# Kernel tuning notes

Hardware: AMD Instinct MI355X
Metric: run time of the kernel (lower is better)

## Reference

```python
import jax, jax.numpy as jnp
import numpy as np
from jax import lax

IOU_THRESHOLD = 0.1
B, N = 4, 8192


def setup_inputs() -> dict:
    key = jax.random.key(0)
    # [B, 5, N]: rows 0..3 = cx, cy, w, h; row 4 = confidence score in (0, 1)
    outputs = jax.random.uniform(key, (B, 5, N), dtype=jnp.float32)
    return {"outputs": outputs}


def _nms_single(p):
    """Greedy NMS on one image. p: [5, N] -> [5, N] with kept boxes
    compacted to the front (original column order preserved) and the rest
    zero-padded. Matches the torch loop: repeatedly take the highest-scoring
    surviving box, drop all boxes with IoU >= threshold (box keeps itself),
    and drop boxes with score <= 0."""
    boxes, scores = p[:4], p[4]
    n = scores.shape[0]
    order = jnp.argsort(-scores)            # descending score order
    b = boxes[:, order]

    x1 = b[0] - b[2] * 0.5
    y1 = b[1] - b[3] * 0.5
    x2 = b[0] + b[2] * 0.5
    y2 = b[1] + b[3] * 0.5
    area = (x2 - x1) * (y2 - y1)

    iw = jnp.clip(jnp.minimum(x2[:, None], x2[None, :]) - jnp.maximum(x1[:, None], x1[None, :]), 0.0)
    ih = jnp.clip(jnp.minimum(y2[:, None], y2[None, :]) - jnp.maximum(y1[:, None], y1[None, :]), 0.0)
    inter = iw * ih
    union = area[:, None] + area[None, :] - inter
    iou = inter / (union + 1e-8)            # [N, N] in sorted order

    idx_range = jnp.arange(n)
    keep_init = scores[order] > 0           # non_zero_scores filter

    def body(i, keep):
        # if box i (in score order) survives, suppress j with IoU >= thr, j != i
        row_keep = (iou[i] < IOU_THRESHOLD) | (idx_range == i)
        return jnp.where(keep[i], keep & row_keep, keep)

    keep_sorted = lax.fori_loop(0, n, body, keep_init)

    # map keep mask back to original column order
    keep_orig = jnp.zeros((n,), bool).at[order].set(keep_sorted)
    # stable compaction: kept columns first, original relative order preserved
    perm = jnp.argsort(jnp.where(keep_orig, 0, 1), stable=True)
    gathered = p[:, perm]                    # [5, N]
    valid = idx_range < jnp.sum(keep_orig)
    return jnp.where(valid[None, :], gathered, 0.0)


def reference(outputs):
    # torch version pads to the max detections across the batch; here we keep
    # the fixed width N (extra columns are zero), same kept values/order.
    return jax.vmap(_nms_single)(outputs)


if __name__ == "__main__":
    inp = setup_inputs()
    out = jax.jit(reference)(**inp)
    print(out.shape, out.dtype)
```

## Files before the change

### kernel.cpp

```cpp
#include <hip/hip_runtime.h>

#pragma clang fp contract(off)

#define NBOX 8192
#define BLK  1024
#define EPT  8
#define NBUCK 2048
#define NB 256
#define IOU_THR 0.1f

typedef unsigned short u16;
typedef unsigned int u32;
typedef unsigned long long u64;

#define MND 0x1.999999p-4

#define SMEM_TOT 160896

__global__ __launch_bounds__(BLK, 4) void nms_kernel(const float* __restrict__ in,
                                                     float* __restrict__ out) {
    __shared__ __align__(16) char smem[SMEM_TOT];
    const int img = blockIdx.x;
    const float* __restrict__ p = in + (size_t)img * 5 * NBOX;
    float* __restrict__ o = out + (size_t)img * 5 * NBOX;
    const int t = threadIdx.x;
    const int lane = t & 63;
    const int wid = t >> 6;

    float4* box   = (float4*)smem;
    u16* A        = (u16*)(smem + 131072);
    float4* bx    = (float4*)(smem + 147456);
    u64 (*mat)[4] = (u64(*)[4])(smem + 151552);
    float4* kx    = (float4*)(smem + 151552);
    u32* pfxA     = (u32*)(smem + 155648);
    u32* kom      = (u32*)(smem + 159744);
    int* wcnt     = (int*)(smem + 160768);
    u64* keptQ    = (u64*)(smem + 160832);
    int* S0sh     = (int*)(smem + 160864);
    u64* skey  = (u64*)smem;
    u32* hist  = (u32*)(smem + 65536);
    u32* bbase = (u32*)(smem + 73728);

    for (int i = t; i < NBUCK; i += BLK) hist[i] = 0;
    if (t < 256) kom[t] = 0;
    if (t == 0) *S0sh = 0;
    __syncthreads();

    u32 mybkt[EPT], myarr[EPT], mykeyhi[EPT];
#pragma unroll
    for (int e = 0; e < EPT; e++) {
        int j = t + e * BLK;
        float s = p[4 * NBOX + j];
        u32 u = __float_as_uint(s);
        u32 ordb = u ^ (u32)(((int)u >> 31) | (int)0x80000000);
        mykeyhi[e] = ~ordb;
        int vb = (int)(s * (float)NBUCK);
        vb = vb < 0 ? 0 : (vb > NBUCK - 1 ? NBUCK - 1 : vb);
        mybkt[e] = (u32)(NBUCK - 1 - vb);
        myarr[e] = atomicAdd(&hist[mybkt[e]], 1u);
        u64 bal = __ballot(s > 0.0f);
        if (lane == 0) atomicAdd(S0sh, (int)__popcll(bal));
    }
    __syncthreads();

    {
        u32 h0 = hist[2 * t], h1 = hist[2 * t + 1];
        int v = (int)(h0 + h1);
        int x = v;
        for (int d = 1; d < 64; d <<= 1) {
            int y = __shfl_up(x, d, 64);
            if (lane >= d) x += y;
        }
        if (lane == 63) wcnt[wid] = x;
        __syncthreads();
        int wb = 0;
        for (int i = 0; i < wid; i++) wb += wcnt[i];
        int excl = wb + x - v;
        bbase[2 * t] = (u32)excl;
        bbase[2 * t + 1] = (u32)excl + h0;
    }
    __syncthreads();

#pragma unroll
    for (int e = 0; e < EPT; e++) {
        u32 pos = bbase[mybkt[e]] + myarr[e];
        skey[pos] = ((u64)mykeyhi[e] << 32) | (u32)(t + e * BLK);
    }
    __syncthreads();

#pragma unroll
    for (int e = 0; e < EPT; e++) {
        u32 b = mybkt[e];
        u32 lo = bbase[b], hi2 = lo + hist[b];
        u64 me = ((u64)mykeyhi[e] << 32) | (u32)(t + e * BLK);
        u32 r = lo;
        for (u32 q = lo; q < hi2; q++) r += (skey[q] < me) ? 1u : 0u;
        A[r] = (u16)(t + e * BLK);
    }
    __syncthreads();
    int S = *S0sh;

#pragma unroll
    for (int e = 0; e < EPT; e++) {
        int j = t + e * BLK;
        float cx = p[j], cy = p[NBOX + j];
        float w_ = p[2 * NBOX + j], h_ = p[3 * NBOX + j];
        box[j] = make_float4(cx - w_ * 0.5f, cy - h_ * 0.5f,
                             cx + w_ * 0.5f, cy + h_ * 0.5f);
    }
    __syncthreads();

    if (t < NB) bx[t] = box[A[t]];
    __syncthreads();

    while (S > 0) {
        int nb = S < NB ? S : NB;

        {
            int i = t >> 2, ws = t & 3;
            if (i < nb) {
                float4 bi = bx[i];
                float ari = (bi.z - bi.x) * (bi.w - bi.y);
                u64 bits = 0;
                int c0 = ws * 64;
                int cmax = nb - c0; if (cmax > 64) cmax = 64;
                for (int cc = 0; cc < cmax; cc++) {
                    float4 bc = bx[c0 + cc];
                    float arc = (bc.z - bc.x) * (bc.w - bc.y);
                    float iw = fmaxf(fminf(bi.z, bc.z) - fmaxf(bi.x, bc.x), 0.0f);
                    float ih = fmaxf(fminf(bi.w, bc.w) - fmaxf(bi.y, bc.y), 0.0f);
                    float inter = iw * ih;
                    float t1 = ari + arc;
                    float t2 = t1 - inter;
                    float u  = t2 + 1e-8f;
                    if ((double)inter > MND * (double)u) bits |= (1ull << cc);
                }
                if (i >= c0 && i < c0 + 64) bits &= ~(1ull << (i - c0));
                mat[i][ws] = bits;
            }
        }
        __syncthreads();

        if (wid == 0) {
            u64 r0[4], r1[4], r2[4], r3[4];
#pragma unroll
            for (int wq = 0; wq < 4; wq++) {
                r0[wq] = mat[lane][wq];
                r1[wq] = mat[64 + lane][wq];
                r2[wq] = mat[128 + lane][wq];
                r3[wq] = mat[192 + lane][wq];
            }
            u64 A0, A1, A2, A3;
            {
                int n0 = nb;       A0 = n0 <= 0 ? 0ull : (n0 >= 64 ? ~0ull : ((1ull << n0) - 1ull));
                int n1 = nb - 64;  A1 = n1 <= 0 ? 0ull : (n1 >= 64 ? ~0ull : ((1ull << n1) - 1ull));
                int n2 = nb - 128; A2 = n2 <= 0 ? 0ull : (n2 >= 64 ? ~0ull : ((1ull << n2) - 1ull));
                int n3 = nb - 192; A3 = n3 <= 0 ? 0ull : (n3 >= 64 ? ~0ull : ((1ull << n3) - 1ull));
            }
            u64 K0 = 0, K1 = 0, K2 = 0, K3 = 0;
            u64 lm = (1ull << lane) - 1ull;
            while (A0 | A1 | A2 | A3) {
                bool c0b = ((A0 >> lane) & 1) && !(r0[0] & A0 & lm);
                bool c1b = ((A1 >> lane) & 1) && !((r1[0] & A0) | (r1[1] & A1 & lm));
                bool c2b = ((A2 >> lane) & 1) && !((r2[0] & A0) | (r2[1] & A1) | (r2[2] & A2 & lm));
                bool c3b = ((A3 >> lane) & 1) && !((r3[0] & A0) | (r3[1] & A1) | (r3[2] & A2) | (r3[3] & A3 & lm));
                u64 C0 = __ballot(c0b), C1 = __ballot(c1b), C2 = __ballot(c2b), C3 = __ballot(c3b);
                K0 |= C0; K1 |= C1; K2 |= C2; K3 |= C3;
                A0 &= ~C0; A1 &= ~C1; A2 &= ~C2; A3 &= ~C3;
                bool s0b = ((A0 >> lane) & 1) && ((r0[0] & C0) | (r0[1] & C1) | (r0[2] & C2) | (r0[3] & C3));
                bool s1b = ((A1 >> lane) & 1) && ((r1[0] & C0) | (r1[1] & C1) | (r1[2] & C2) | (r1[3] & C3));
                bool s2b = ((A2 >> lane) & 1) && ((r2[0] & C0) | (r2[1] & C1) | (r2[2] & C2) | (r2[3] & C3));
                bool s3b = ((A3 >> lane) & 1) && ((r3[0] & C0) | (r3[1] & C1) | (r3[2] & C2) | (r3[3] & C3));
                A0 &= ~__ballot(s0b); A1 &= ~__ballot(s1b); A2 &= ~__ballot(s2b); A3 &= ~__ballot(s3b);
            }
            if (lane < 4) keptQ[lane] = lane == 0 ? K0 : lane == 1 ? K1 : lane == 2 ? K2 : K3;
        }
        __syncthreads();

        u64 kq0 = keptQ[0], kq1 = keptQ[1], kq2 = keptQ[2], kq3 = keptQ[3];
        int nk = (int)(__popcll(kq0) + __popcll(kq1) + __popcll(kq2) + __popcll(kq3));
        if (t < nb) {
            int wq = t >> 6;
            u64 kq = wq == 0 ? kq0 : wq == 1 ? kq1 : wq == 2 ? kq2 : kq3;
            if ((kq >> (t & 63)) & 1) {
                int j = (int)A[t];
                atomicOr(&kom[j >> 5], 1u << (j & 31));
                int pk = 0;
                if (wq > 0) pk += (int)__popcll(kq0);
                if (wq > 1) pk += (int)__popcll(kq1);
                if (wq > 2) pk += (int)__popcll(kq2);
                pk += (int)__popcll(kq & ((1ull << (t & 63)) - 1ull));
                kx[pk] = bx[t];
            }
        }
        int tailN = S - nb;
        int C = (tailN + BLK - 1) / BLK;
        int st = nb + t * C;
        int en = st + C; if (en > S) en = S;
        float4 eb[EPT]; float ea[EPT]; u16 ei[EPT];
        u32 am = 0;
#pragma unroll
        for (int e = 0; e < EPT; e++) {
            int pos = st + e;
            if (e < C && pos < en) {
                u16 j = A[pos];
                ei[e] = j;
                float4 b = box[j];
                eb[e] = b;
                ea[e] = (b.z - b.x) * (b.w - b.y);
                am |= (1u << e);
            }
        }
        __syncthreads();

        if (am) {
            for (int c = 0; c < nk; c++) {
                float4 cb = kx[c];
                float arc = (cb.z - cb.x) * (cb.w - cb.y);
#pragma unroll
                for (int e = 0; e < EPT; e++) {
                    if (am & (1u << e)) {
                        float iw = fminf(eb[e].z, cb.z) - fmaxf(eb[e].x, cb.x);
                        float ih = fminf(eb[e].w, cb.w) - fmaxf(eb[e].y, cb.y);
                        if (iw > 0.0f && ih > 0.0f) {
                            float inter = iw * ih;
                            float t1 = ea[e] + arc;
                            float t2 = t1 - inter;
                            float u  = t2 + 1e-8f;
                            if ((double)inter > MND * (double)u) am &= ~(1u << e);
                        }
                    }
                }
                if (!am) break;
            }
        }

        {
            int cnt = __popc(am);
            int x = cnt;
            for (int d = 1; d < 64; d <<= 1) {
                int y = __shfl_up(x, d, 64);
                if (lane >= d) x += y;
            }
            if (lane == 63) wcnt[wid] = x;
            __syncthreads();
            int wb = 0, tot = 0;
            for (int i = 0; i < BLK / 64; i++) {
                int v = wcnt[i];
                if (i < wid) wb += v;
                tot += v;
            }
            int off = wb + x - cnt;
#pragma unroll
            for (int e = 0; e < EPT; e++) {
                if (am & (1u << e)) {
                    A[off] = ei[e];
                    if (off < NB) bx[off] = eb[e];
                    off++;
                }
            }
            __syncthreads();
            S = tot;
        }
    }
    __syncthreads();

    {
        float4 z; z.x = z.y = z.z = z.w = 0.0f;
        float4* o4 = (float4*)o;
        for (int i = t; i < 5 * NBOX / 4; i += BLK) o4[i] = z;
    }
    {
        u32 w = (t < 256) ? kom[t] : 0u;
        int c = __popc(w);
        int x = c;
        for (int d = 1; d < 64; d <<= 1) {
            int y = __shfl_up(x, d, 64);
            if (lane >= d) x += y;
        }
        if (lane == 63) wcnt[wid] = x;
        __syncthreads();
        int wb = 0;
        for (int i = 0; i < wid; i++) wb += wcnt[i];
        if (t < 256) pfxA[t] = (u32)(wb + x - c);
    }
    __syncthreads();
    for (int j = t; j < NBOX; j += BLK) {
        u32 km = kom[j >> 5];
        if ((km >> (j & 31)) & 1u) {
            int pos = (int)(pfxA[j >> 5] + (u32)__popc(km & ((1u << (j & 31)) - 1u)));
            o[0 * NBOX + pos] = p[0 * NBOX + j];
            o[1 * NBOX + pos] = p[1 * NBOX + j];
            o[2 * NBOX + pos] = p[2 * NBOX + j];
            o[3 * NBOX + pos] = p[3 * NBOX + j];
            o[4 * NBOX + pos] = p[4 * NBOX + j];
        }
    }
}

extern "C" void kernel_launch(void* const* d_in, const int* in_sizes, int n_in,
                              void* d_out, int out_size, void* d_ws, size_t ws_size,
                              hipStream_t stream) {
    const float* in = (const float*)d_in[0];
    float* out = (float*)d_out;
    int B = in_sizes[0] / (5 * NBOX);
    hipLaunchKernelGGL(nms_kernel, dim3(B), dim3(BLK), 0, stream, in, out);
}
```

Baseline: 162.2 us.

## Overlap tail loading with wave-0 greedy resolve and compute only lower-triangle IoU bits

```diff
diff --git a/kernel.cpp b/kernel.cpp
--- a/kernel.cpp
+++ b/kernel.cpp
@@ -4,7 +4,7 @@
 
 #define NBOX 8192
 #define BLK  1024
-#define EPT  8
+#define EPT2 9
 #define NBUCK 2048
 #define NB 256
 #define IOU_THR 0.1f
@@ -41,14 +41,21 @@
     u32* hist  = (u32*)(smem + 65536);
     u32* bbase = (u32*)(smem + 73728);
 
+    {
+        float4 z; z.x = z.y = z.z = z.w = 0.0f;
+        float4* o4 = (float4*)o;
+#pragma unroll
+        for (int e = 0; e < 10; e++) o4[t + e * BLK] = z;
+    }
+
     for (int i = t; i < NBUCK; i += BLK) hist[i] = 0;
     if (t < 256) kom[t] = 0;
     if (t == 0) *S0sh = 0;
     __syncthreads();
 
-    u32 mybkt[EPT], myarr[EPT], mykeyhi[EPT];
-#pragma unroll
-    for (int e = 0; e < EPT; e++) {
+    u32 mybkt[8], myarr[8], mykeyhi[8];
+#pragma unroll
+    for (int e = 0; e < 8; e++) {
         int j = t + e * BLK;
         float s = p[4 * NBOX + j];
         u32 u = __float_as_uint(s);
@@ -82,14 +89,14 @@
     __syncthreads();
 
 #pragma unroll
-    for (int e = 0; e < EPT; e++) {
+    for (int e = 0; e < 8; e++) {
         u32 pos = bbase[mybkt[e]] + myarr[e];
         skey[pos] = ((u64)mykeyhi[e] << 32) | (u32)(t + e * BLK);
     }
     __syncthreads();
 
 #pragma unroll
-    for (int e = 0; e < EPT; e++) {
+    for (int e = 0; e < 8; e++) {
         u32 b = mybkt[e];
         u32 lo = bbase[b], hi2 = lo + hist[b];
         u64 me = ((u64)mykeyhi[e] << 32) | (u32)(t + e * BLK);
@@ -101,7 +108,7 @@
     int S = *S0sh;
 
 #pragma unroll
-    for (int e = 0; e < EPT; e++) {
+    for (int e = 0; e < 8; e++) {
         int j = t + e * BLK;
         float cx = p[j], cy = p[NBOX + j];
         float w_ = p[2 * NBOX + j], h_ = p[3 * NBOX + j];
@@ -119,28 +126,32 @@
         {
             int i = t >> 2, ws = t & 3;
             if (i < nb) {
-                float4 bi = bx[i];
-                float ari = (bi.z - bi.x) * (bi.w - bi.y);
+                int c0 = ws * 64;
+                int lim = i - c0; if (lim > 64) lim = 64;
                 u64 bits = 0;
-                int c0 = ws * 64;
-                int cmax = nb - c0; if (cmax > 64) cmax = 64;
-                for (int cc = 0; cc < cmax; cc++) {
-                    float4 bc = bx[c0 + cc];
-                    float arc = (bc.z - bc.x) * (bc.w - bc.y);
-                    float iw = fmaxf(fminf(bi.z, bc.z) - fmaxf(bi.x, bc.x), 0.0f);
-                    float ih = fmaxf(fminf(bi.w, bc.w) - fmaxf(bi.y, bc.y), 0.0f);
-                    float inter = iw * ih;
-                    float t1 = ari + arc;
-                    float t2 = t1 - inter;
-                    float u  = t2 + 1e-8f;
-                    if ((double)inter > MND * (double)u) bits |= (1ull << cc);
+                if (lim > 0) {
+                    float4 bi = bx[i];
+                    float ari = (bi.z - bi.x) * (bi.w - bi.y);
+                    for (int cc = 0; cc < lim; cc++) {
+                        float4 bc = bx[c0 + cc];
+                        float arc = (bc.z - bc.x) * (bc.w - bc.y);
+                        float iw = fmaxf(fminf(bi.z, bc.z) - fmaxf(bi.x, bc.x), 0.0f);
+                        float ih = fmaxf(fminf(bi.w, bc.w) - fmaxf(bi.y, bc.y), 0.0f);
+                        float inter = iw * ih;
+                        float t2 = (ari + arc) - inter;
+                        float u  = t2 + 1e-8f;
+                        if ((double)inter > MND * (double)u) bits |= (1ull << cc);
+                    }
                 }
-                if (i >= c0 && i < c0 + 64) bits &= ~(1ull << (i - c0));
                 mat[i][ws] = bits;
             }
         }
         __syncthreads();
 
+        int tailN = S - nb;
+        int C = tailN > 0 ? (tailN + 959) / 960 : 0;
+        float4 eb[EPT2]; float ea[EPT2]; u16 ei[EPT2];
+        u32 am = 0;
         if (wid == 0) {
             u64 r0[4], r1[4], r2[4], r3[4];
 #pragma unroll
@@ -174,6 +185,21 @@
                 A0 &= ~__ballot(s0b); A1 &= ~__ballot(s1b); A2 &= ~__ballot(s2b); A3 &= ~__ballot(s3b);
             }
             if (lane < 4) keptQ[lane] = lane == 0 ? K0 : lane == 1 ? K1 : lane == 2 ? K2 : K3;
+        } else {
+            int ti = t - 64;
+            int st = nb + ti * C;
+#pragma unroll
+            for (int e = 0; e < EPT2; e++) {
+                int pos = st + e;
+                if (e < C && pos < S) {
+                    u16 j = A[pos];
+                    ei[e] = j;
+                    float4 b = box[j];
+                    eb[e] = b;
+                    ea[e] = (b.z - b.x) * (b.w - b.y);
+                    am |= (1u << e);
+                }
+            }
         }
         __syncthreads();
 
@@ -193,24 +219,6 @@
                 kx[pk] = bx[t];
             }
         }
-        int tailN = S - nb;
-        int C = (tailN + BLK - 1) / BLK;
-        int st = nb + t * C;
-        int en = st + C; if (en > S) en = S;
-        float4 eb[EPT]; float ea[EPT]; u16 ei[EPT];
-        u32 am = 0;
-#pragma unroll
-        for (int e = 0; e < EPT; e++) {
-            int pos = st + e;
-            if (e < C && pos < en) {
-                u16 j = A[pos];
-                ei[e] = j;
-                float4 b = box[j];
-                eb[e] = b;
-                ea[e] = (b.z - b.x) * (b.w - b.y);
-                am |= (1u << e);
-            }
-        }
         __syncthreads();
 
         if (am) {
@@ -218,14 +226,13 @@
                 float4 cb = kx[c];
                 float arc = (cb.z - cb.x) * (cb.w - cb.y);
 #pragma unroll
-                for (int e = 0; e < EPT; e++) {
+                for (int e = 0; e < EPT2; e++) {
                     if (am & (1u << e)) {
                         float iw = fminf(eb[e].z, cb.z) - fmaxf(eb[e].x, cb.x);
                         float ih = fminf(eb[e].w, cb.w) - fmaxf(eb[e].y, cb.y);
                         if (iw > 0.0f && ih > 0.0f) {
                             float inter = iw * ih;
-                            float t1 = ea[e] + arc;
-                            float t2 = t1 - inter;
+                            float t2 = (ea[e] + arc) - inter;
                             float u  = t2 + 1e-8f;
                             if ((double)inter > MND * (double)u) am &= ~(1u << e);
                         }
@@ -252,7 +259,7 @@
             }
             int off = wb + x - cnt;
 #pragma unroll
-            for (int e = 0; e < EPT; e++) {
+            for (int e = 0; e < EPT2; e++) {
                 if (am & (1u << e)) {
                     A[off] = ei[e];
                     if (off < NB) bx[off] = eb[e];
@@ -265,11 +272,6 @@
     }
     __syncthreads();
 
-    {
-        float4 z; z.x = z.y = z.z = z.w = 0.0f;
-        float4* o4 = (float4*)o;
-        for (int i = t; i < 5 * NBOX / 4; i += BLK) o4[i] = z;
-    }
     {
         u32 w = (t < 256) ? kom[t] : 0u;
         int c = __popc(w);
```

Result: slower. 171.6 us (+5.8%).
